# Optimization experiments

Measured on AMD Instinct MI355X. Metric: run time of the kernel, lower is better.

## Reference

```python
import jax, jax.numpy as jnp
import numpy as np

B, T, DIM, H = 4, 2048, 1024, 16
HD = DIM // H  # 64
ROPE_BASE = 10000.0


def _rope_cos_sin(seq_len, head_dim, dtype):
    # lucidrains rotary-embedding-torch convention: interleaved pairs.
    inv_freq = 1.0 / (ROPE_BASE ** (jnp.arange(0, head_dim, 2, dtype=jnp.float32) / head_dim))
    freqs = jnp.arange(seq_len, dtype=jnp.float32)[:, None] * inv_freq[None, :]  # [T, hd/2]
    freqs = jnp.repeat(freqs, 2, axis=-1)  # [T, hd], each freq duplicated for the pair
    return jnp.cos(freqs).astype(dtype), jnp.sin(freqs).astype(dtype)


def _rotate_half(x):
    # interleaved pairs: (x1, x2) -> (-x2, x1)
    x = x.reshape(*x.shape[:-1], -1, 2)
    x1, x2 = x[..., 0], x[..., 1]
    return jnp.stack([-x2, x1], axis=-1).reshape(*x.shape[:-2], -1)


def _apply_rope(x, cos, sin):
    # x: [B, H, T, hd]; cos/sin: [T, hd]
    return x * cos[None, None, :, :] + _rotate_half(x) * sin[None, None, :, :]


def setup_inputs() -> dict:
    key = jax.random.key(0)
    kx, kqkv, kw, kb = jax.random.split(key, 4)
    s_qkv = 1.0 / np.sqrt(DIM)
    return {
        "x": jax.random.normal(kx, (B, T, DIM), dtype=jnp.float32),
        "w_qkv": jax.random.normal(kqkv, (3 * DIM, DIM), dtype=jnp.float32) * s_qkv,
        "w_proj": jax.random.normal(kw, (DIM, DIM), dtype=jnp.float32) * s_qkv,
        "b_proj": jax.random.normal(kb, (DIM,), dtype=jnp.float32) * 0.01,
    }


def reference(x, w_qkv, w_proj, b_proj):
    b, t, c = x.shape
    qkv = jnp.einsum('btc,dc->btd', x, w_qkv)  # [B, T, 3*C]
    qkv = qkv.reshape(b, t, 3, H, HD).transpose(2, 0, 3, 1, 4)  # [3, B, H, T, hd]
    q, k, v = qkv[0], qkv[1], qkv[2]

    cos, sin = _rope_cos_sin(t, HD, x.dtype)
    q = _apply_rope(q, cos, sin)
    k = _apply_rope(k, cos, sin)

    scale = 1.0 / np.sqrt(HD)
    scores = jnp.einsum('bhqd,bhkd->bhqk', q, k) * scale  # [B, H, T, T]
    attn = jax.nn.softmax(scores, axis=-1)
    out = jnp.einsum('bhqk,bhkd->bhqd', attn, v)  # [B, H, T, hd]

    out = out.transpose(0, 2, 1, 3).reshape(b, t, c)  # [B, T, C]
    return jnp.einsum('btc,dc->btd', out, w_proj) + b_proj
```

## Files before the change

### kernel.cpp

```cpp
#include <hip/hip_runtime.h>
#include <hip/hip_bf16.h>
#include <math.h>

#define Bz   4
#define Tz   2048
#define DIMz 1024
#define Hz   16
#define HDz  64
#define BHz  (Bz*Hz)
#define Mz   (Bz*Tz)
#define LOG2E 1.44269504088896340736f
#define QSCALE (0.125f * LOG2E)

typedef __attribute__((ext_vector_type(8))) __bf16 bf16x8;
typedef __attribute__((ext_vector_type(4))) __bf16 bf16x4;
typedef __attribute__((ext_vector_type(4))) float  f32x4;

__device__ __forceinline__ f32x4 mfma_16x16x32(bf16x8 a, bf16x8 b, f32x4 c) {
  return __builtin_amdgcn_mfma_f32_16x16x32_bf16(a, b, c, 0, 0, 0);
}

__device__ __forceinline__ ushort f2bf(float f) {
  unsigned u = __float_as_uint(f);
  u += 0x7fffu + ((u >> 16) & 1u);
  return (ushort)(u >> 16);
}
__device__ __forceinline__ float bf2f(ushort h) {
  return __uint_as_float(((unsigned)h) << 16);
}

__device__ __forceinline__ void gl_lds16(const ushort* g, ushort* l) {
  __builtin_amdgcn_global_load_lds(
      (const __attribute__((address_space(1))) unsigned int*)g,
      (__attribute__((address_space(3))) unsigned int*)l, 16, 0, 0);
}

__global__ void k_cvt(const float4* __restrict__ in, ushort4* __restrict__ out, int n4) {
  int i = blockIdx.x * blockDim.x + threadIdx.x;
  if (i >= n4) return;
  float4 v = in[i];
  ushort4 o;
  o.x = f2bf(v.x); o.y = f2bf(v.y); o.z = f2bf(v.z); o.w = f2bf(v.w);
  out[i] = o;
}

__global__ void k_rope_tab(float* __restrict__ tab) {
  int idx = blockIdx.x * blockDim.x + threadIdx.x;
  if (idx >= Tz * 32) return;
  int t = idx >> 5, i = idx & 31;
  double ang = (double)t * exp(((double)(-2 * i) / (double)HDz) * log(10000.0));
  tab[2 * idx]     = (float)cos(ang);
  tab[2 * idx + 1] = (float)sin(ang);
}


__global__ __launch_bounds__(256) void k_gemm_qkv(const ushort* __restrict__ A,
                                                  const ushort* __restrict__ Bw,
                                                  const float* __restrict__ tab,
                                                  ushort* __restrict__ qb,
                                                  ushort* __restrict__ kb,
                                                  ushort* __restrict__ vbt) {
  __shared__ ushort As[128 * 64];
  __shared__ ushort Bs[128 * 64];
  const int tid = threadIdx.x;
  const int bm = (blockIdx.x & 63) << 7;
  const int bn = (blockIdx.x >> 6) << 7;
  const int wid = tid >> 6, lane = tid & 63;
  const int wr = (wid & 1) << 6, wc = (wid >> 1) << 6;
  const int lr = lane & 15, lg = lane >> 4;

  const int r8 = lane >> 3;
  const int cswz = (((lane & 7) ^ r8) << 3);
  const ushort* pA = A  + (size_t)(bm + wid * 8 + r8) * 1024 + cswz;
  const ushort* pB = Bw + (size_t)(bn + wid * 8 + r8) * 1024 + cswz;
  ushort* lA = &As[wid * 512];
  ushort* lB = &Bs[wid * 512];

  const int cs0 = ((lg ^ (lr & 7)) << 3);
  const int cs1 = cs0 ^ 32;

  const f32x4 fz = {0.f, 0.f, 0.f, 0.f};
  f32x4 acc[4][4];
  #pragma unroll
  for (int i = 0; i < 4; i++)
    #pragma unroll
    for (int j = 0; j < 4; j++) acc[i][j] = fz;

  for (int k0 = 0; k0 < 1024; k0 += 64) {
    __syncthreads();
    #pragma unroll
    for (int rep = 0; rep < 4; rep++) {
      gl_lds16(pA + (size_t)rep * 32768 + k0, lA + rep * 2048);
      gl_lds16(pB + (size_t)rep * 32768 + k0, lB + rep * 2048);
    }
    __syncthreads();
    #pragma unroll
    for (int kc = 0; kc < 2; kc++) {
      const int cs = kc ? cs1 : cs0;
      bf16x8 af[4], bfr[4];
      #pragma unroll
      for (int i = 0; i < 4; i++)
        af[i] = *reinterpret_cast<const bf16x8*>(&As[(wr + i * 16 + lr) * 64 + cs]);
      #pragma unroll
      for (int j = 0; j < 4; j++)
        bfr[j] = *reinterpret_cast<const bf16x8*>(&Bs[(wc + j * 16 + lr) * 64 + cs]);
      #pragma unroll
      for (int i = 0; i < 4; i++)
        #pragma unroll
        for (int j = 0; j < 4; j++)
          acc[i][j] = mfma_16x16x32(af[i], bfr[j], acc[i][j]);
    }
  }

  #pragma unroll
  for (int j = 0; j < 4; j++) {
    int col = bn + wc + j * 16 + lr;
    int which = col >> 10;
    int r = col & 1023;
    int h = r >> 6, hd = r & 63;
    #pragma unroll
    for (int i = 0; i < 4; i++) {
      int row0 = bm + wr + i * 16 + lg * 4;
      int b = row0 >> 11, t0 = row0 & 2047;
      if (which == 2) {
        uint lo = (uint)f2bf(acc[i][j][0]) | ((uint)f2bf(acc[i][j][1]) << 16);
        uint hi = (uint)f2bf(acc[i][j][2]) | ((uint)f2bf(acc[i][j][3]) << 16);
        *reinterpret_cast<uint2*>(&vbt[((size_t)(b * Hz + h) * HDz + hd) * Tz + t0]) =
            make_uint2(lo, hi);
      } else {
        ushort* dst = (which == 0) ? qb : kb;
        const float sc = (which == 0) ? QSCALE : 1.0f;
        const float sgn = (hd & 1) ? 1.0f : -1.0f;
        const float* tb = &tab[((size_t)t0 * 32 + (hd >> 1)) * 2];
        #pragma unroll
        for (int q = 0; q < 4; q++) {
          float own = acc[i][j][q];
          float other = __shfl_xor(own, 1);
          float c = tb[q * 64], s = tb[q * 64 + 1];
          dst[(((size_t)(b * Hz + h) * Tz + t0 + q) << 6) + hd] =
              f2bf((own * c + sgn * other * s) * sc);
        }
      }
    }
  }
}

__global__ __launch_bounds__(256, 4) void k_attn(const ushort* __restrict__ qb,
                                                 const ushort* __restrict__ kb,
                                                 const ushort* __restrict__ vbt,
                                                 ushort* __restrict__ ao) {
  __shared__ ushort Ks[2][64 * 64];
  __shared__ ushort Vs[2][64 * 64];
  __shared__ ushort Ps[4][16 * 64];

  const int bid = ((blockIdx.x & 7) << 7) + (blockIdx.x >> 3);
  const int qt = bid & 15;
  const int bh = bid >> 4;
  const int tid = threadIdx.x, wid = tid >> 6, lane = tid & 63;
  const int lr = lane & 15, lg = lane >> 4;

  const ushort* Qg = qb + ((size_t)bh * Tz + qt * 128 + wid * 32) * HDz;
  const ushort* Kg = kb + (size_t)bh * Tz * HDz;
  const ushort* Vg = vbt + (size_t)bh * HDz * Tz;

  bf16x8 qA0 = *reinterpret_cast<const bf16x8*>(&Qg[lr * 64 + lg * 8]);
  bf16x8 qA1 = *reinterpret_cast<const bf16x8*>(&Qg[lr * 64 + lg * 8 + 32]);
  bf16x8 qB0 = *reinterpret_cast<const bf16x8*>(&Qg[(16 + lr) * 64 + lg * 8]);
  bf16x8 qB1 = *reinterpret_cast<const bf16x8*>(&Qg[(16 + lr) * 64 + lg * 8 + 32]);

  bf16x8 onev;
  #pragma unroll
  for (int j = 0; j < 8; j++) onev[j] = (__bf16)1.0f;

  const int r8 = lane >> 3;
  const int cswz = (((lane & 7) ^ r8) << 3);
  const ushort* kb0 = Kg + (size_t)(wid * 16 + r8) * 64 + cswz;
  const ushort* kb1 = kb0 + 8 * 64;
  const ushort* vb0 = Vg + (size_t)(wid * 16 + r8) * Tz + cswz;
  const ushort* vb1 = vb0 + (size_t)8 * Tz;

  const f32x4 fz = {0.f, 0.f, 0.f, 0.f};
  f32x4 oaccA[4], oaccB[4];
  #pragma unroll
  for (int db = 0; db < 4; db++) { oaccA[db] = fz; oaccB[db] = fz; }
  f32x4 laccA = fz, laccB = fz;

  const int cs0 = ((lg ^ (lr & 7)) << 3);
  const int cs1 = cs0 ^ 32;
  const int swz8 = (lr & 7) << 3;

  {
    ushort* kl = &Ks[0][wid * 1024];
    ushort* vl = &Vs[0][wid * 1024];
    gl_lds16(kb0, kl); gl_lds16(kb1, kl + 512);
    gl_lds16(vb0, vl); gl_lds16(vb1, vl + 512);
  }
  __syncthreads();

  int cur = 0;
  for (int kt = 0; kt < Tz / 64; kt++) {
    if (kt + 1 < Tz / 64) {
      ushort* kl = &Ks[cur ^ 1][wid * 1024];
      ushort* vl = &Vs[cur ^ 1][wid * 1024];
      gl_lds16(kb0 + (size_t)(kt + 1) * 4096, kl);
      gl_lds16(kb1 + (size_t)(kt + 1) * 4096, kl + 512);
      gl_lds16(vb0 + (kt + 1) * 64, vl);
      gl_lds16(vb1 + (kt + 1) * 64, vl + 512);
    }

    f32x4 stA[4], stB[4];
    __builtin_amdgcn_s_setprio(1);
    #pragma unroll
    for (int nb = 0; nb < 4; nb++) {
      const ushort* kp = &Ks[cur][(nb * 16 + lr) * 64];
      bf16x8 kf0 = *reinterpret_cast<const bf16x8*>(kp + cs0);
      bf16x8 kf1 = *reinterpret_cast<const bf16x8*>(kp + cs1);
      stA[nb] = mfma_16x16x32(kf0, qA0, fz);
      stA[nb] = mfma_16x16x32(kf1, qA1, stA[nb]);
      stB[nb] = mfma_16x16x32(kf0, qB0, fz);
      stB[nb] = mfma_16x16x32(kf1, qB1, stB[nb]);
    }
    __builtin_amdgcn_s_setprio(0);

    bf16x4 pa[4], pbv[4];
    #pragma unroll
    for (int nb = 0; nb < 4; nb++) {
      #pragma unroll
      for (int r = 0; r < 4; r++) {
        pa[nb][r]  = (__bf16)__builtin_exp2f(stA[nb][r]);
        pbv[nb][r] = (__bf16)__builtin_exp2f(stB[nb][r]);
      }
    }

    #pragma unroll
    for (int nb = 0; nb < 4; nb++)
      *reinterpret_cast<bf16x4*>(&Ps[wid][lr * 64 + ((16 * nb + 4 * lg) ^ swz8)]) = pa[nb];
    asm volatile("s_waitcnt lgkmcnt(0)" ::: "memory");
    const ushort* pp = &Ps[wid][lr * 64];
    bf16x8 pfA0 = *reinterpret_cast<const bf16x8*>(pp + cs0);
    bf16x8 pfA1 = *reinterpret_cast<const bf16x8*>(pp + cs1);

    #pragma unroll
    for (int nb = 0; nb < 4; nb++)
      *reinterpret_cast<bf16x4*>(&Ps[wid][lr * 64 + ((16 * nb + 4 * lg) ^ swz8)]) = pbv[nb];
    asm volatile("s_waitcnt lgkmcnt(0)" ::: "memory");
    bf16x8 pfB0 = *reinterpret_cast<const bf16x8*>(pp + cs0);
    bf16x8 pfB1 = *reinterpret_cast<const bf16x8*>(pp + cs1);

    __builtin_amdgcn_s_setprio(1);
    laccA = mfma_16x16x32(pfA0, onev, laccA);
    laccA = mfma_16x16x32(pfA1, onev, laccA);
    laccB = mfma_16x16x32(pfB0, onev, laccB);
    laccB = mfma_16x16x32(pfB1, onev, laccB);
    #pragma unroll
    for (int db = 0; db < 4; db++) {
      const ushort* vp = &Vs[cur][(db * 16 + lr) * 64];
      bf16x8 vf0 = *reinterpret_cast<const bf16x8*>(vp + cs0);
      bf16x8 vf1 = *reinterpret_cast<const bf16x8*>(vp + cs1);
      oaccA[db] = mfma_16x16x32(pfA0, vf0, oaccA[db]);
      oaccA[db] = mfma_16x16x32(pfA1, vf1, oaccA[db]);
      oaccB[db] = mfma_16x16x32(pfB0, vf0, oaccB[db]);
      oaccB[db] = mfma_16x16x32(pfB1, vf1, oaccB[db]);
    }
    __builtin_amdgcn_s_setprio(0);

    __syncthreads();
    cur ^= 1;
  }

  const int b = bh >> 4, h = bh & 15;
  #pragma unroll
  for (int r = 0; r < 4; r++) {
    float invA = 1.0f / laccA[r];
    float invB = 1.0f / laccB[r];
    int tA = qt * 128 + wid * 32 + lg * 4 + r;
    size_t baseA = ((size_t)(b * Tz + tA) * Hz + h) * HDz;
    size_t baseB = ((size_t)(b * Tz + tA + 16) * Hz + h) * HDz;
    #pragma unroll
    for (int db = 0; db < 4; db++) {
      ao[baseA + db * 16 + lr] = f2bf(oaccA[db][r] * invA);
      ao[baseB + db * 16 + lr] = f2bf(oaccB[db][r] * invB);
    }
  }
}

__global__ __launch_bounds__(256) void k_gemm_proj(const ushort* __restrict__ A,
                                                   const ushort* __restrict__ Bw,
                                                   const float* __restrict__ bias,
                                                   float* __restrict__ out) {
  __shared__ ushort As[128 * 64];
  __shared__ ushort Bs[128 * 64];
  const int tid = threadIdx.x;
  const int bm = (blockIdx.x & 63) << 7;
  const int bn = (blockIdx.x >> 6) << 7;
  const int wid = tid >> 6, lane = tid & 63;
  const int wr = (wid & 1) << 6, wc = (wid >> 1) << 6;
  const int lr = lane & 15, lg = lane >> 4;

  const int r8 = lane >> 3;
  const int cswz = (((lane & 7) ^ r8) << 3);
  const ushort* pA = A  + (size_t)(bm + wid * 8 + r8) * 1024 + cswz;
  const ushort* pB = Bw + (size_t)(bn + wid * 8 + r8) * 1024 + cswz;
  ushort* lA = &As[wid * 512];
  ushort* lB = &Bs[wid * 512];

  const int cs0 = ((lg ^ (lr & 7)) << 3);
  const int cs1 = cs0 ^ 32;

  const f32x4 fz = {0.f, 0.f, 0.f, 0.f};
  f32x4 acc[4][4];
  #pragma unroll
  for (int i = 0; i < 4; i++)
    #pragma unroll
    for (int j = 0; j < 4; j++) acc[i][j] = fz;

  for (int k0 = 0; k0 < 1024; k0 += 64) {
    __syncthreads();
    #pragma unroll
    for (int rep = 0; rep < 4; rep++) {
      gl_lds16(pA + (size_t)rep * 32768 + k0, lA + rep * 2048);
      gl_lds16(pB + (size_t)rep * 32768 + k0, lB + rep * 2048);
    }
    __syncthreads();
    #pragma unroll
    for (int kc = 0; kc < 2; kc++) {
      const int cs = kc ? cs1 : cs0;
      bf16x8 af[4], bfr[4];
      #pragma unroll
      for (int i = 0; i < 4; i++)
        af[i] = *reinterpret_cast<const bf16x8*>(&As[(wr + i * 16 + lr) * 64 + cs]);
      #pragma unroll
      for (int j = 0; j < 4; j++)
        bfr[j] = *reinterpret_cast<const bf16x8*>(&Bs[(wc + j * 16 + lr) * 64 + cs]);
      #pragma unroll
      for (int i = 0; i < 4; i++)
        #pragma unroll
        for (int j = 0; j < 4; j++)
          acc[i][j] = mfma_16x16x32(af[i], bfr[j], acc[i][j]);
    }
  }

  #pragma unroll
  for (int j = 0; j < 4; j++) {
    int col = bn + wc + j * 16 + lr;
    float bv = bias[col];
    #pragma unroll
    for (int i = 0; i < 4; i++) {
      #pragma unroll
      for (int q = 0; q < 4; q++) {
        int row = bm + wr + i * 16 + lg * 4 + q;
        out[(size_t)row * 1024 + col] = acc[i][j][q] + bv;
      }
    }
  }
}

extern "C" void kernel_launch(void* const* d_in, const int* in_sizes, int n_in,
                              void* d_out, int out_size, void* d_ws, size_t ws_size,
                              hipStream_t stream) {
  const float* x      = (const float*)d_in[0];
  const float* w_qkv  = (const float*)d_in[1];
  const float* w_proj = (const float*)d_in[2];
  const float* b_proj = (const float*)d_in[3];
  float* out = (float*)d_out;

  char* ws = (char*)d_ws;
  ushort* xh     = (ushort*)ws; ws += (size_t)Mz * DIMz * 2;
  ushort* wqkvh  = (ushort*)ws; ws += (size_t)3 * DIMz * DIMz * 2;
  ushort* wprojh = (ushort*)ws; ws += (size_t)DIMz * DIMz * 2;
  ushort* qbuf   = (ushort*)ws; ws += (size_t)BHz * Tz * HDz * 2;
  ushort* kbuf   = (ushort*)ws; ws += (size_t)BHz * Tz * HDz * 2;
  ushort* vbuft  = (ushort*)ws; ws += (size_t)BHz * HDz * Tz * 2;
  ushort* aout   = (ushort*)ws; ws += (size_t)Mz * DIMz * 2;
  float*  tab    = (float*)ws;  ws += (size_t)Tz * 32 * 2 * 4;

  k_cvt<<<8192, 256, 0, stream>>>((const float4*)x,      (ushort4*)xh,     Mz * DIMz / 4);
  k_cvt<<<3072, 256, 0, stream>>>((const float4*)w_qkv,  (ushort4*)wqkvh,  3 * DIMz * DIMz / 4);
  k_cvt<<<1024, 256, 0, stream>>>((const float4*)w_proj, (ushort4*)wprojh, DIMz * DIMz / 4);
  k_rope_tab<<<256, 256, 0, stream>>>(tab);
  k_gemm_qkv<<<64 * 24, 256, 0, stream>>>(xh, wqkvh, tab, qbuf, kbuf, vbuft);
  k_attn<<<BHz * (Tz / 128), 256, 0, stream>>>(qbuf, kbuf, vbuft, aout);
  k_gemm_proj<<<64 * 8, 256, 0, stream>>>(aout, wprojh, b_proj, out);
}
```

Before: 215.0 us.

## Switch attention kernel to 32x32x16 MFMA with register-shuffled P fragments

Rewrites the attention inner loop to use 32x32x16 bf16 MFMA tiles instead of 16x16x32, so each wave computes its 32 query rows against 64 keys with fewer, larger matrix instructions. The probability tile is now moved between the two half-waves with cross-lane shuffles rather than being staged through an LDS scratch buffer, which removes the Ps shared array along with its writes, reads and waits. The LDS swizzle for K and V is reworked to match the new fragment layout. The trade-off is larger accumulators and more register pressure under the 4-waves launch bound, plus select/shuffle ALU work.

Measured after the change: 225.5 us. +4.9%, slower.

```diff
diff --git a/kernel.cpp b/kernel.cpp
--- a/kernel.cpp
+++ b/kernel.cpp
@@ -12,12 +12,17 @@
 #define LOG2E 1.44269504088896340736f
 #define QSCALE (0.125f * LOG2E)
 
-typedef __attribute__((ext_vector_type(8))) __bf16 bf16x8;
-typedef __attribute__((ext_vector_type(4))) __bf16 bf16x4;
-typedef __attribute__((ext_vector_type(4))) float  f32x4;
+typedef __attribute__((ext_vector_type(8)))  __bf16 bf16x8;
+typedef __attribute__((ext_vector_type(4)))  __bf16 bf16x4;
+typedef __attribute__((ext_vector_type(2)))  __bf16 bf16x2;
+typedef __attribute__((ext_vector_type(4)))  float  f32x4;
+typedef __attribute__((ext_vector_type(16))) float  f32x16;
 
 __device__ __forceinline__ f32x4 mfma_16x16x32(bf16x8 a, bf16x8 b, f32x4 c) {
   return __builtin_amdgcn_mfma_f32_16x16x32_bf16(a, b, c, 0, 0, 0);
+}
+__device__ __forceinline__ f32x16 mfma_32x32x16(bf16x8 a, bf16x8 b, f32x16 c) {
+  return __builtin_amdgcn_mfma_f32_32x32x16_bf16(a, b, c, 0, 0, 0);
 }
 
 __device__ __forceinline__ ushort f2bf(float f) {
@@ -146,54 +151,55 @@
 }
 
 __global__ __launch_bounds__(256, 4) void k_attn(const ushort* __restrict__ qb,
-                                                 const ushort* __restrict__ kb,
+                                                 const ushort* __restrict__ kbp,
                                                  const ushort* __restrict__ vbt,
                                                  ushort* __restrict__ ao) {
   __shared__ ushort Ks[2][64 * 64];
   __shared__ ushort Vs[2][64 * 64];
-  __shared__ ushort Ps[4][16 * 64];
 
   const int bid = ((blockIdx.x & 7) << 7) + (blockIdx.x >> 3);
   const int qt = bid & 15;
   const int bh = bid >> 4;
   const int tid = threadIdx.x, wid = tid >> 6, lane = tid & 63;
-  const int lr = lane & 15, lg = lane >> 4;
-
-  const ushort* Qg = qb + ((size_t)bh * Tz + qt * 128 + wid * 32) * HDz;
-  const ushort* Kg = kb + (size_t)bh * Tz * HDz;
+  const int l31 = lane & 31, hi = lane >> 5;
+
+  const ushort* Kg = kbp + (size_t)bh * Tz * HDz;
   const ushort* Vg = vbt + (size_t)bh * HDz * Tz;
 
-  bf16x8 qA0 = *reinterpret_cast<const bf16x8*>(&Qg[lr * 64 + lg * 8]);
-  bf16x8 qA1 = *reinterpret_cast<const bf16x8*>(&Qg[lr * 64 + lg * 8 + 32]);
-  bf16x8 qB0 = *reinterpret_cast<const bf16x8*>(&Qg[(16 + lr) * 64 + lg * 8]);
-  bf16x8 qB1 = *reinterpret_cast<const bf16x8*>(&Qg[(16 + lr) * 64 + lg * 8 + 32]);
+  const ushort* Qrow = qb + ((size_t)bh * Tz + qt * 128 + wid * 32 + l31) * HDz + hi * 8;
+  bf16x8 qf[4];
+  #pragma unroll
+  for (int m = 0; m < 4; m++)
+    qf[m] = *reinterpret_cast<const bf16x8*>(Qrow + m * 16);
 
   bf16x8 onev;
   #pragma unroll
   for (int j = 0; j < 8; j++) onev[j] = (__bf16)1.0f;
 
   const int r8 = lane >> 3;
-  const int cswz = (((lane & 7) ^ r8) << 3);
-  const ushort* kb0 = Kg + (size_t)(wid * 16 + r8) * 64 + cswz;
-  const ushort* kb1 = kb0 + 8 * 64;
-  const ushort* vb0 = Vg + (size_t)(wid * 16 + r8) * Tz + cswz;
-  const ushort* vb1 = vb0 + (size_t)8 * Tz;
-
-  const f32x4 fz = {0.f, 0.f, 0.f, 0.f};
-  f32x4 oaccA[4], oaccB[4];
-  #pragma unroll
-  for (int db = 0; db < 4; db++) { oaccA[db] = fz; oaccB[db] = fz; }
-  f32x4 laccA = fz, laccB = fz;
-
-  const int cs0 = ((lg ^ (lr & 7)) << 3);
-  const int cs1 = cs0 ^ 32;
-  const int swz8 = (lr & 7) << 3;
+  const int c0 = (((lane & 7) ^ r8 ^ ((2 * wid) & 3)) << 3);
+  const int c1 = (((lane & 7) ^ r8 ^ ((2 * wid + 1) & 3)) << 3);
+  const ushort* kp0 = Kg + (size_t)(wid * 16 + r8) * 64 + c0;
+  const ushort* kp1 = Kg + (size_t)(wid * 16 + 8 + r8) * 64 + c1;
+  const ushort* vp0 = Vg + (size_t)(wid * 16 + r8) * Tz + c0;
+  const ushort* vp1 = Vg + (size_t)(wid * 16 + 8 + r8) * Tz + c1;
+
+  f32x16 oacc0, oacc1, lacc;
+  #pragma unroll
+  for (int i = 0; i < 16; i++) { oacc0[i] = 0.f; oacc1[i] = 0.f; lacc[i] = 0.f; }
+
+  const int swr = (lane & 7) ^ ((lane >> 3) & 3);
+  int csk[4];
+  #pragma unroll
+  for (int m = 0; m < 4; m++) csk[m] = ((2 * m + hi) ^ swr) << 3;
+
+  union U8 { uint u[4]; bf16x8 v; };
 
   {
     ushort* kl = &Ks[0][wid * 1024];
     ushort* vl = &Vs[0][wid * 1024];
-    gl_lds16(kb0, kl); gl_lds16(kb1, kl + 512);
-    gl_lds16(vb0, vl); gl_lds16(vb1, vl + 512);
+    gl_lds16(kp0, kl); gl_lds16(kp1, kl + 512);
+    gl_lds16(vp0, vl); gl_lds16(vp1, vl + 512);
   }
   __syncthreads();
 
@@ -202,65 +208,73 @@
     if (kt + 1 < Tz / 64) {
       ushort* kl = &Ks[cur ^ 1][wid * 1024];
       ushort* vl = &Vs[cur ^ 1][wid * 1024];
-      gl_lds16(kb0 + (size_t)(kt + 1) * 4096, kl);
-      gl_lds16(kb1 + (size_t)(kt + 1) * 4096, kl + 512);
-      gl_lds16(vb0 + (kt + 1) * 64, vl);
-      gl_lds16(vb1 + (kt + 1) * 64, vl + 512);
-    }
-
-    f32x4 stA[4], stB[4];
+      gl_lds16(kp0 + (size_t)(kt + 1) * 4096, kl);
+      gl_lds16(kp1 + (size_t)(kt + 1) * 4096, kl + 512);
+      gl_lds16(vp0 + (kt + 1) * 64, vl);
+      gl_lds16(vp1 + (kt + 1) * 64, vl + 512);
+    }
+
+    f32x16 sA, sB;
+    #pragma unroll
+    for (int i = 0; i < 16; i++) { sA[i] = 0.f; sB[i] = 0.f; }
     __builtin_amdgcn_s_setprio(1);
     #pragma unroll
-    for (int nb = 0; nb < 4; nb++) {
-      const ushort* kp = &Ks[cur][(nb * 16 + lr) * 64];
-      bf16x8 kf0 = *reinterpret_cast<const bf16x8*>(kp + cs0);
-      bf16x8 kf1 = *reinterpret_cast<const bf16x8*>(kp + cs1);
-      stA[nb] = mfma_16x16x32(kf0, qA0, fz);
-      stA[nb] = mfma_16x16x32(kf1, qA1, stA[nb]);
-      stB[nb] = mfma_16x16x32(kf0, qB0, fz);
-      stB[nb] = mfma_16x16x32(kf1, qB1, stB[nb]);
+    for (int m = 0; m < 4; m++) {
+      bf16x8 kfA = *reinterpret_cast<const bf16x8*>(&Ks[cur][l31 * 64 + csk[m]]);
+      bf16x8 kfB = *reinterpret_cast<const bf16x8*>(&Ks[cur][(32 + l31) * 64 + csk[m]]);
+      sA = mfma_32x32x16(kfA, qf[m], sA);
+      sB = mfma_32x32x16(kfB, qf[m], sB);
     }
     __builtin_amdgcn_s_setprio(0);
 
-    bf16x4 pa[4], pbv[4];
-    #pragma unroll
-    for (int nb = 0; nb < 4; nb++) {
-      #pragma unroll
-      for (int r = 0; r < 4; r++) {
-        pa[nb][r]  = (__bf16)__builtin_exp2f(stA[nb][r]);
-        pbv[nb][r] = (__bf16)__builtin_exp2f(stB[nb][r]);
-      }
-    }
-
-    #pragma unroll
-    for (int nb = 0; nb < 4; nb++)
-      *reinterpret_cast<bf16x4*>(&Ps[wid][lr * 64 + ((16 * nb + 4 * lg) ^ swz8)]) = pa[nb];
-    asm volatile("s_waitcnt lgkmcnt(0)" ::: "memory");
-    const ushort* pp = &Ps[wid][lr * 64];
-    bf16x8 pfA0 = *reinterpret_cast<const bf16x8*>(pp + cs0);
-    bf16x8 pfA1 = *reinterpret_cast<const bf16x8*>(pp + cs1);
-
-    #pragma unroll
-    for (int nb = 0; nb < 4; nb++)
-      *reinterpret_cast<bf16x4*>(&Ps[wid][lr * 64 + ((16 * nb + 4 * lg) ^ swz8)]) = pbv[nb];
-    asm volatile("s_waitcnt lgkmcnt(0)" ::: "memory");
-    bf16x8 pfB0 = *reinterpret_cast<const bf16x8*>(pp + cs0);
-    bf16x8 pfB1 = *reinterpret_cast<const bf16x8*>(pp + cs1);
+    uint pkA[8], pkB[8];
+    #pragma unroll
+    for (int i = 0; i < 8; i++) {
+      bf16x2 ta, tb2;
+      ta[0]  = (__bf16)__builtin_exp2f(sA[2 * i]);
+      ta[1]  = (__bf16)__builtin_exp2f(sA[2 * i + 1]);
+      tb2[0] = (__bf16)__builtin_exp2f(sB[2 * i]);
+      tb2[1] = (__bf16)__builtin_exp2f(sB[2 * i + 1]);
+      pkA[i] = *reinterpret_cast<uint*>(&ta);
+      pkB[i] = *reinterpret_cast<uint*>(&tb2);
+    }
+
+    uint eA0 = __shfl_xor(hi ? pkA[0] : pkA[2], 32);
+    uint eA1 = __shfl_xor(hi ? pkA[1] : pkA[3], 32);
+    uint eA2 = __shfl_xor(hi ? pkA[4] : pkA[6], 32);
+    uint eA3 = __shfl_xor(hi ? pkA[5] : pkA[7], 32);
+    uint eB0 = __shfl_xor(hi ? pkB[0] : pkB[2], 32);
+    uint eB1 = __shfl_xor(hi ? pkB[1] : pkB[3], 32);
+    uint eB2 = __shfl_xor(hi ? pkB[4] : pkB[6], 32);
+    uint eB3 = __shfl_xor(hi ? pkB[5] : pkB[7], 32);
+    U8 fA0, fA1, fB0, fB1;
+    fA0.u[0] = hi ? eA0 : pkA[0]; fA0.u[1] = hi ? eA1 : pkA[1];
+    fA0.u[2] = hi ? pkA[2] : eA0; fA0.u[3] = hi ? pkA[3] : eA1;
+    fA1.u[0] = hi ? eA2 : pkA[4]; fA1.u[1] = hi ? eA3 : pkA[5];
+    fA1.u[2] = hi ? pkA[6] : eA2; fA1.u[3] = hi ? pkA[7] : eA3;
+    fB0.u[0] = hi ? eB0 : pkB[0]; fB0.u[1] = hi ? eB1 : pkB[1];
+    fB0.u[2] = hi ? pkB[2] : eB0; fB0.u[3] = hi ? pkB[3] : eB1;
+    fB1.u[0] = hi ? eB2 : pkB[4]; fB1.u[1] = hi ? eB3 : pkB[5];
+    fB1.u[2] = hi ? pkB[6] : eB2; fB1.u[3] = hi ? pkB[7] : eB3;
 
     __builtin_amdgcn_s_setprio(1);
-    laccA = mfma_16x16x32(pfA0, onev, laccA);
-    laccA = mfma_16x16x32(pfA1, onev, laccA);
-    laccB = mfma_16x16x32(pfB0, onev, laccB);
-    laccB = mfma_16x16x32(pfB1, onev, laccB);
-    #pragma unroll
-    for (int db = 0; db < 4; db++) {
-      const ushort* vp = &Vs[cur][(db * 16 + lr) * 64];
-      bf16x8 vf0 = *reinterpret_cast<const bf16x8*>(vp + cs0);
-      bf16x8 vf1 = *reinterpret_cast<const bf16x8*>(vp + cs1);
-      oaccA[db] = mfma_16x16x32(pfA0, vf0, oaccA[db]);
-      oaccA[db] = mfma_16x16x32(pfA1, vf1, oaccA[db]);
-      oaccB[db] = mfma_16x16x32(pfB0, vf0, oaccB[db]);
-      oaccB[db] = mfma_16x16x32(pfB1, vf1, oaccB[db]);
+    lacc = mfma_32x32x16(fA0.v, onev, lacc);
+    lacc = mfma_32x32x16(fA1.v, onev, lacc);
+    lacc = mfma_32x32x16(fB0.v, onev, lacc);
+    lacc = mfma_32x32x16(fB1.v, onev, lacc);
+    #pragma unroll
+    for (int blk = 0; blk < 2; blk++) {
+      const ushort* vrow = &Vs[cur][(blk * 32 + l31) * 64];
+      bf16x8 vf0 = *reinterpret_cast<const bf16x8*>(vrow + csk[0]);
+      bf16x8 vf1 = *reinterpret_cast<const bf16x8*>(vrow + csk[1]);
+      bf16x8 vf2 = *reinterpret_cast<const bf16x8*>(vrow + csk[2]);
+      bf16x8 vf3 = *reinterpret_cast<const bf16x8*>(vrow + csk[3]);
+      f32x16 o = blk ? oacc1 : oacc0;
+      o = mfma_32x32x16(fA0.v, vf0, o);
+      o = mfma_32x32x16(fA1.v, vf1, o);
+      o = mfma_32x32x16(fB0.v, vf2, o);
+      o = mfma_32x32x16(fB1.v, vf3, o);
+      if (blk) oacc1 = o; else oacc0 = o;
     }
     __builtin_amdgcn_s_setprio(0);
 
@@ -270,17 +284,13 @@
 
   const int b = bh >> 4, h = bh & 15;
   #pragma unroll
-  for (int r = 0; r < 4; r++) {
-    float invA = 1.0f / laccA[r];
-    float invB = 1.0f / laccB[r];
-    int tA = qt * 128 + wid * 32 + lg * 4 + r;
-    size_t baseA = ((size_t)(b * Tz + tA) * Hz + h) * HDz;
-    size_t baseB = ((size_t)(b * Tz + tA + 16) * Hz + h) * HDz;
-    #pragma unroll
-    for (int db = 0; db < 4; db++) {
-      ao[baseA + db * 16 + lr] = f2bf(oaccA[db][r] * invA);
-      ao[baseB + db * 16 + lr] = f2bf(oaccB[db][r] * invB);
-    }
+  for (int r = 0; r < 16; r++) {
+    int qrow = (r & 3) + 8 * (r >> 2) + 4 * hi;
+    int t = qt * 128 + wid * 32 + qrow;
+    float inv = 1.0f / lacc[r];
+    size_t base = ((size_t)(b * Tz + t) * Hz + h) * HDz;
+    ao[base + l31]      = f2bf(oacc0[r] * inv);
+    ao[base + 32 + l31] = f2bf(oacc1[r] * inv);
   }
 }
 
```
